# Kernel optimization log

Measured on AMD Instinct MI355X. Metric: run time of the kernel, lower is better.

## Reference

```python
import jax, jax.numpy as jnp
import numpy as np

B, S, E, H, F, V = 4, 2048, 1024, 16, 4096, 32000
D = E // H  # head_dim = 64
LN_EPS = 1e-5


def layer_norm(x, g, b):
    mu = jnp.mean(x, axis=-1, keepdims=True)
    var = jnp.mean(jnp.square(x - mu), axis=-1, keepdims=True)
    return (x - mu) * jax.lax.rsqrt(var + LN_EPS) * g + b


def setup_inputs() -> dict:
    key = jax.random.key(0)
    ks = jax.random.split(key, 12)
    s = 0.02
    return {
        "input_ids": jax.random.randint(ks[0], (B, S), 0, V),
        "attention_mask": jnp.ones((B, S), dtype=jnp.int32),
        "emb_table": jax.random.normal(ks[1], (V, E), jnp.float32) * s,
        "Wq": jax.random.normal(ks[2], (E, E), jnp.float32) * s,
        "bq": jnp.zeros((E,), jnp.float32),
        "Wk": jax.random.normal(ks[3], (E, E), jnp.float32) * s,
        "bk": jnp.zeros((E,), jnp.float32),
        "Wv": jax.random.normal(ks[4], (E, E), jnp.float32) * s,
        "bv": jnp.zeros((E,), jnp.float32),
        "Wo": jax.random.normal(ks[5], (E, E), jnp.float32) * s,
        "bo": jnp.zeros((E,), jnp.float32),
        "ln_g": jnp.ones((E,), jnp.float32),
        "ln_b": jnp.zeros((E,), jnp.float32),
        "W1": jax.random.normal(ks[6], (E, F), jnp.float32) * s,
        "b1": jnp.zeros((F,), jnp.float32),
        "W2": jax.random.normal(ks[7], (F, E), jnp.float32) * s,
        "b2": jnp.zeros((E,), jnp.float32),
        "Wp": jax.random.normal(ks[8], (E, 3), jnp.float32) * s,
        "bp": jnp.zeros((3,), jnp.float32),
    }


def reference(input_ids, attention_mask, emb_table, Wq, bq, Wk, bk, Wv, bv,
              Wo, bo, ln_g, ln_b, W1, b1, W2, b2, Wp, bp):
    b, s = input_ids.shape
    x = emb_table[input_ids]                                  # [B,S,E]
    q = (x @ Wq + bq).reshape(b, s, H, D).transpose(0, 2, 1, 3)  # [B,H,S,D]
    k = (x @ Wk + bk).reshape(b, s, H, D).transpose(0, 2, 1, 3)
    v = (x @ Wv + bv).reshape(b, s, H, D).transpose(0, 2, 1, 3)
    scores = jnp.einsum('bhqd,bhkd->bhqk', q, k) / jnp.sqrt(jnp.float32(D))
    mask = attention_mask[:, None, None, :]                   # [B,1,1,S]
    scores = jnp.where(mask == 0, -jnp.inf, scores)
    attn = jax.nn.softmax(scores, axis=-1)
    ctx = jnp.einsum('bhqk,bhkd->bhqd', attn, v)              # [B,H,S,D]
    ctx = ctx.transpose(0, 2, 1, 3).reshape(b, s, E)
    ctx = ctx @ Wo + bo
    h = layer_norm(ctx + x, ln_g, ln_b)
    ff = jax.nn.gelu(h @ W1 + b1, approximate=False) @ W2 + b2
    logits = ff @ Wp + bp                                     # [B,S,3]
    return logits.mean(axis=1)                                # [B,3]
```

## Files before the change

### kernel.cpp

```cpp
#include <hip/hip_runtime.h>
#include <hip/hip_bf16.h>
#include <math.h>

#define BB 4
#define SS 2048
#define EE 1024
#define HH 16
#define DD 64
#define FF 4096

typedef unsigned short u16;
typedef unsigned int u32;
typedef __bf16 bf16x8 __attribute__((ext_vector_type(8)));
typedef float f32x4 __attribute__((ext_vector_type(4)));

static __device__ __forceinline__ float gelu_exact(float v){
  return 0.5f * v * (1.0f + erff(v * 0.70710678118654752f));
}

static __device__ __forceinline__ u16 f2bf(float f){
  union { float f; u32 u; } x; x.f = f;
  u32 r = x.u + 0x7FFFu + ((x.u >> 16) & 1u);
  return (u16)(r >> 16);
}
static __device__ __forceinline__ void unpack2(u32 u, float& lo, float& hi){
  union { u32 u; float f; } a, b;
  a.u = u << 16; b.u = u & 0xFFFF0000u;
  lo = a.f; hi = b.f;
}

#define GLOAD_LDS16(g, l) \
  __builtin_amdgcn_global_load_lds((const __attribute__((address_space(1))) void*)(g), \
      (__attribute__((address_space(3))) void*)(l), 16, 0, 0)

__global__ __launch_bounds__(256) void embed_kernel(const int* __restrict__ ids,
    const float* __restrict__ emb, float* __restrict__ xf, u16* __restrict__ xbf){
  int row = blockIdx.x;
  int id  = ids[row];
  float4 v = ((const float4*)(emb + (size_t)id * EE))[threadIdx.x];
  ((float4*)(xf + (size_t)row * EE))[threadIdx.x] = v;
  ushort4 u; u.x = f2bf(v.x); u.y = f2bf(v.y); u.z = f2bf(v.z); u.w = f2bf(v.w);
  ((ushort4*)(xbf + (size_t)row * EE))[threadIdx.x] = u;
}

__global__ __launch_bounds__(256) void prep_weights(const float* __restrict__ Wq,
    const float* __restrict__ Wk, const float* __restrict__ Wv,
    const float* __restrict__ Wo, const float* __restrict__ W1, u16* __restrict__ WT){
  __shared__ float tile[32][33];
  int bid = blockIdx.x;
  const float* W; u16* dst; int N, n0, k0;
  if (bid < 4096){
    W = W1; dst = WT + (size_t)4 * EE * EE; N = FF;
    n0 = (bid & 127) * 32; k0 = (bid >> 7) * 32;
  } else {
    int idx = bid - 4096;
    int which = idx >> 10, t = idx & 1023;
    W = (which == 0) ? Wq : (which == 1) ? Wk : (which == 2) ? Wv : Wo;
    dst = WT + (size_t)which * EE * EE; N = EE;
    n0 = (t & 31) * 32; k0 = (t >> 5) * 32;
  }
  int tx = threadIdx.x & 31, ty = threadIdx.x >> 5;
  #pragma unroll
  for (int i = 0; i < 4; i++)
    tile[ty + 8*i][tx] = W[(size_t)(k0 + ty + 8*i) * N + n0 + tx];
  __syncthreads();
  #pragma unroll
  for (int i = 0; i < 4; i++)
    dst[(size_t)(n0 + ty + 8*i) * EE + k0 + tx] = f2bf(tile[tx][ty + 8*i]);
}

template<int MODE>
__global__ __launch_bounds__(256) void gemm_mfma(const u16* __restrict__ A,
    const u16* __restrict__ WT, const float* __restrict__ bias,
    const float* __restrict__ biasB, const float* __restrict__ biasC,
    u16* __restrict__ C, float* __restrict__ gsum, int M, int N, int K){
  __shared__ __attribute__((aligned(16))) u16 As[128 * 32];
  __shared__ __attribute__((aligned(16))) u16 Bs[128 * 32];

  const int tid = threadIdx.x;
  const int l = tid & 63, w = tid >> 6;
  const int lm = l & 15, lq = l >> 4;
  const int wm = (w >> 1) * 64, wn = (w & 1) * 64;
  const int r0 = blockIdx.y * 128, c0 = blockIdx.x * 128;

  const int srow0 = w * 32 + (l >> 2);
  const int scol  = (l & 3) * 8;
  const u16* Ab = A  + (size_t)(r0 + srow0) * K + scol;
  const u16* Bb = WT + (size_t)(c0 + srow0) * K + scol;
  u16* AsBase0 = &As[(w * 2)     * 512];
  u16* AsBase1 = &As[(w * 2 + 1) * 512];
  u16* BsBase0 = &Bs[(w * 2)     * 512];
  u16* BsBase1 = &Bs[(w * 2 + 1) * 512];

  f32x4 acc[4][4];
  const f32x4 zero = {0.f, 0.f, 0.f, 0.f};
  #pragma unroll
  for (int mi = 0; mi < 4; mi++)
    #pragma unroll
    for (int ni = 0; ni < 4; ni++) acc[mi][ni] = zero;

  for (int k0 = 0; k0 < K; k0 += 32){
    GLOAD_LDS16(Ab + k0,                    AsBase0);
    GLOAD_LDS16(Ab + (size_t)16 * K + k0,   AsBase1);
    GLOAD_LDS16(Bb + k0,                    BsBase0);
    GLOAD_LDS16(Bb + (size_t)16 * K + k0,   BsBase1);
    __syncthreads();

    bf16x8 af[4], bf[4];
    #pragma unroll
    for (int mi = 0; mi < 4; mi++)
      af[mi] = *(const bf16x8*)&As[(wm + mi*16 + lm) * 32 + lq * 8];
    #pragma unroll
    for (int ni = 0; ni < 4; ni++)
      bf[ni] = *(const bf16x8*)&Bs[(wn + ni*16 + lm) * 32 + lq * 8];
    #pragma unroll
    for (int mi = 0; mi < 4; mi++)
      #pragma unroll
      for (int ni = 0; ni < 4; ni++)
        acc[mi][ni] = __builtin_amdgcn_mfma_f32_16x16x32_bf16(af[mi], bf[ni], acc[mi][ni], 0, 0, 0);
    __syncthreads();
  }

  if constexpr (MODE == 0){
    #pragma unroll
    for (int ni = 0; ni < 4; ni++){
      int col = c0 + wn + ni*16 + lm;
      float bcol = bias[col];
      #pragma unroll
      for (int mi = 0; mi < 4; mi++){
        #pragma unroll
        for (int r = 0; r < 4; r++){
          int row = r0 + wm + mi*16 + lq*4 + r;
          C[(size_t)row * N + col] = f2bf(acc[mi][ni][r] + bcol);
        }
      }
    }
  } else if constexpr (MODE == 2){
    #pragma unroll
    for (int ni = 0; ni < 4; ni++){
      int col3 = c0 + wn + ni*16 + lm;
      int sel  = col3 >> 10;
      int colm = col3 & 1023;
      const float* bp_ = (sel == 0) ? bias : ((sel == 1) ? biasB : biasC);
      float bcol = bp_[colm];
      u16* dst = C + (size_t)sel * ((size_t)M * N);
      #pragma unroll
      for (int mi = 0; mi < 4; mi++){
        #pragma unroll
        for (int r = 0; r < 4; r++){
          int row = r0 + wm + mi*16 + lq*4 + r;
          dst[(size_t)row * N + colm] = f2bf(acc[mi][ni][r] + bcol);
        }
      }
    }
  } else {
    const int batch = r0 >> 11;
    #pragma unroll
    for (int ni = 0; ni < 4; ni++){
      int col = c0 + wn + ni*16 + lm;
      float bcol = bias[col];
      float cs = 0.f;
      #pragma unroll
      for (int mi = 0; mi < 4; mi++)
        #pragma unroll
        for (int r = 0; r < 4; r++)
          cs += gelu_exact(acc[mi][ni][r] + bcol);
      cs += __shfl_xor(cs, 16, 64);
      cs += __shfl_xor(cs, 32, 64);
      if (lq == 0) atomicAdd(&gsum[(size_t)batch * N + col], cs);
    }
  }
}

__global__ __launch_bounds__(256, 4) void attn_mfma(const u16* __restrict__ q,
    const u16* __restrict__ k, const u16* __restrict__ v,
    const int* __restrict__ mask, u16* __restrict__ ctx){
  const int bh = blockIdx.y, b = bh >> 4, h = bh & 15;
  const int q0 = blockIdx.x * 128;
  const int tid = threadIdx.x;
  const int w = tid >> 6, l = tid & 63, lm = l & 15, lq = l >> 4;

  __shared__ __attribute__((aligned(16))) u16 Kt[64 * 72];
  __shared__ __attribute__((aligned(16))) u16 Vt[64 * 72];
  __shared__ __attribute__((aligned(16))) u16 Pw[4][32 * 72];
  __shared__ float mb[64];

  bf16x8 aq[2][2];
  #pragma unroll
  for (int mg = 0; mg < 2; mg++){
    const u16* qrow = q + (size_t)(b*SS + q0 + w*32 + mg*16 + lm) * EE + h*DD + lq*8;
    aq[mg][0] = *(const bf16x8*)qrow;
    aq[mg][1] = *(const bf16x8*)(qrow + 32);
  }

  f32x4 occ[2][4];
  const f32x4 zero = {0.f,0.f,0.f,0.f};
  #pragma unroll
  for (int mg = 0; mg < 2; mg++)
    #pragma unroll
    for (int ni = 0; ni < 4; ni++) occ[mg][ni] = zero;
  float l_part[2][4] = {{0.f,0.f,0.f,0.f},{0.f,0.f,0.f,0.f}};

  const int kkey = tid >> 2, kc16 = (tid & 3) * 16;
  const u16* kbase = k + (size_t)(b*SS + kkey) * EE + h*DD + kc16;
  const int kp = tid & 31, vd0 = (tid >> 5) * 8;
  const u16* vbase0 = v + (size_t)(b*SS + 2*kp) * EE + h*DD + vd0;
  const u16* vbase1 = vbase0 + EE;

  uint4 kr0 = *(const uint4*)(kbase);
  uint4 kr1 = *(const uint4*)(kbase + 8);
  uint4 vr0 = *(const uint4*)(vbase0);
  uint4 vr1 = *(const uint4*)(vbase1);
  float mreg = 0.f;
  if (tid < 64) mreg = (mask[b*SS + tid] != 0) ? 0.f : -1e30f;

  const float SCALE_LOG2E = 0.125f * 1.4426950408889634f;

  for (int t0 = 0; t0 < SS; t0 += 64){
    *(uint4*)&Kt[kkey*72 + kc16]     = kr0;
    *(uint4*)&Kt[kkey*72 + kc16 + 8] = kr1;
    {
      union { uint4 u; u16 s[8]; } va, vb;
      va.u = vr0; vb.u = vr1;
      #pragma unroll
      for (int i = 0; i < 8; i++){
        u32 pk = (u32)va.s[i] | ((u32)vb.s[i] << 16);
        *(u32*)&Vt[(vd0 + i)*72 + 2*kp] = pk;
      }
    }
    if (tid < 64) mb[tid] = mreg;
    __syncthreads();

    if (t0 + 64 < SS){
      kr0 = *(const uint4*)(kbase + (size_t)(t0 + 64) * EE);
      kr1 = *(const uint4*)(kbase + (size_t)(t0 + 64) * EE + 8);
      vr0 = *(const uint4*)(vbase0 + (size_t)(t0 + 64) * EE);
      vr1 = *(const uint4*)(vbase1 + (size_t)(t0 + 64) * EE);
      if (tid < 64) mreg = (mask[b*SS + t0 + 64 + tid] != 0) ? 0.f : -1e30f;
    }

    #pragma unroll
    for (int mg = 0; mg < 2; mg++){
      #pragma unroll
      for (int ni = 0; ni < 4; ni++){
        bf16x8 b0 = *(const bf16x8*)&Kt[(ni*16 + lm)*72 + lq*8];
        bf16x8 b1 = *(const bf16x8*)&Kt[(ni*16 + lm)*72 + 32 + lq*8];
        f32x4 sc = zero;
        sc = __builtin_amdgcn_mfma_f32_16x16x32_bf16(aq[mg][0], b0, sc, 0, 0, 0);
        sc = __builtin_amdgcn_mfma_f32_16x16x32_bf16(aq[mg][1], b1, sc, 0, 0, 0);
        float mbias = mb[ni*16 + lm];
        #pragma unroll
        for (int r = 0; r < 4; r++){
          float s = fminf(fmaf(sc[r], SCALE_LOG2E, mbias), 80.f);
          float p = __builtin_amdgcn_exp2f(s);
          l_part[mg][r] += p;
          Pw[w][(mg*16 + lq*4 + r)*72 + ni*16 + lm] = f2bf(p);
        }
      }
    }
    bf16x8 ap[2][2];
    #pragma unroll
    for (int mg = 0; mg < 2; mg++){
      ap[mg][0] = *(const bf16x8*)&Pw[w][(mg*16 + lm)*72 + lq*8];
      ap[mg][1] = *(const bf16x8*)&Pw[w][(mg*16 + lm)*72 + 32 + lq*8];
    }

    #pragma unroll
    for (int ni = 0; ni < 4; ni++){
      bf16x8 vb0 = *(const bf16x8*)&Vt[(ni*16 + lm)*72 + lq*8];
      bf16x8 vb1 = *(const bf16x8*)&Vt[(ni*16 + lm)*72 + 32 + lq*8];
      #pragma unroll
      for (int mg = 0; mg < 2; mg++){
        occ[mg][ni] = __builtin_amdgcn_mfma_f32_16x16x32_bf16(ap[mg][0], vb0, occ[mg][ni], 0, 0, 0);
        occ[mg][ni] = __builtin_amdgcn_mfma_f32_16x16x32_bf16(ap[mg][1], vb1, occ[mg][ni], 0, 0, 0);
      }
    }
    __syncthreads();
  }

  #pragma unroll
  for (int mg = 0; mg < 2; mg++){
    float inv[4];
    #pragma unroll
    for (int r = 0; r < 4; r++){
      float s = l_part[mg][r];
      s += __shfl_xor(s, 1, 64);
      s += __shfl_xor(s, 2, 64);
      s += __shfl_xor(s, 4, 64);
      s += __shfl_xor(s, 8, 64);
      inv[r] = 1.f / s;
    }
    #pragma unroll
    for (int ni = 0; ni < 4; ni++){
      int col = h*DD + ni*16 + lm;
      #pragma unroll
      for (int r = 0; r < 4; r++){
        int row = q0 + w*32 + mg*16 + lq*4 + r;
        ctx[(size_t)(b*SS + row) * EE + col] = f2bf(occ[mg][ni][r] * inv[r]);
      }
    }
  }
}

__global__ __launch_bounds__(256) void ln_kernel(const u16* __restrict__ c2,
    const float* __restrict__ x, const float* __restrict__ g,
    const float* __restrict__ bta, u16* __restrict__ h){
  int row = blockIdx.x, tid = threadIdx.x;
  uint2 cu = ((const uint2*)(c2 + (size_t)row * EE))[tid];
  float c0,c1,c2f,c3;
  unpack2(cu.x, c0, c1); unpack2(cu.y, c2f, c3);
  float4 xv = ((const float4*)(x + (size_t)row * EE))[tid];
  float4 y = make_float4(c0+xv.x, c1+xv.y, c2f+xv.z, c3+xv.w);
  float s  = y.x + y.y + y.z + y.w;
  float ss = y.x*y.x + y.y*y.y + y.z*y.z + y.w*y.w;
  #pragma unroll
  for (int off=32; off; off>>=1){
    s  += __shfl_xor(s,  off, 64);
    ss += __shfl_xor(ss, off, 64);
  }
  __shared__ float rs[4], rss[4];
  int w = tid >> 6;
  if ((tid & 63) == 0){ rs[w] = s; rss[w] = ss; }
  __syncthreads();
  float tot  = rs[0]+rs[1]+rs[2]+rs[3];
  float tots = rss[0]+rss[1]+rss[2]+rss[3];
  float mu  = tot  * (1.f/EE);
  float var = tots * (1.f/EE) - mu*mu;
  float inv = rsqrtf(var + 1e-5f);
  float4 gv = ((const float4*)g)[tid];
  float4 bv = ((const float4*)bta)[tid];
  ushort4 ou;
  ou.x = f2bf((y.x-mu)*inv*gv.x + bv.x);
  ou.y = f2bf((y.y-mu)*inv*gv.y + bv.y);
  ou.z = f2bf((y.z-mu)*inv*gv.z + bv.z);
  ou.w = f2bf((y.w-mu)*inv*gv.w + bv.w);
  ((ushort4*)(h + (size_t)row * EE))[tid] = ou;
}

__global__ __launch_bounds__(256) void w2wp_kernel(const float* __restrict__ W2,
    const float* __restrict__ Wp, float* __restrict__ W2Wp){
  int f0 = blockIdx.x * 8;
  int tid = threadIdx.x;
  int e0 = tid * 4;
  float wp[4][3];
  #pragma unroll
  for (int t = 0; t < 4; t++)
    #pragma unroll
    for (int j = 0; j < 3; j++) wp[t][j] = Wp[(e0 + t)*3 + j];
  __shared__ float red[3][4];
  for (int i = 0; i < 8; i++){
    int f = f0 + i;
    float4 wv = ((const float4*)(W2 + (size_t)f * EE))[tid];
    float w4[4] = {wv.x, wv.y, wv.z, wv.w};
    float p[3] = {0.f, 0.f, 0.f};
    #pragma unroll
    for (int t = 0; t < 4; t++)
      #pragma unroll
      for (int j = 0; j < 3; j++) p[j] += w4[t] * wp[t][j];
    #pragma unroll
    for (int j = 0; j < 3; j++){
      float sj = p[j];
      #pragma unroll
      for (int off = 32; off; off >>= 1) sj += __shfl_xor(sj, off, 64);
      if ((tid & 63) == 0) red[j][tid >> 6] = sj;
    }
    __syncthreads();
    if (tid < 3) W2Wp[f*3 + tid] = red[tid][0] + red[tid][1] + red[tid][2] + red[tid][3];
    __syncthreads();
  }
}

__global__ __launch_bounds__(256) void out_final(const float* __restrict__ gsum,
    const float* __restrict__ W2Wp, const float* __restrict__ b2,
    const float* __restrict__ Wp, const float* __restrict__ bp, float* __restrict__ out){
  int tid = threadIdx.x;
  float part[4][3];
  #pragma unroll
  for (int b = 0; b < 4; b++)
    #pragma unroll
    for (int j = 0; j < 3; j++) part[b][j] = 0.f;
  for (int f = tid; f < FF; f += 256){
    float w0 = W2Wp[f*3], w1 = W2Wp[f*3+1], w2v = W2Wp[f*3+2];
    #pragma unroll
    for (int b = 0; b < 4; b++){
      float g = gsum[b*FF + f] * (1.f/SS);
      part[b][0] += g * w0; part[b][1] += g * w1; part[b][2] += g * w2v;
    }
  }
  float bb[3] = {0.f, 0.f, 0.f};
  for (int e = tid; e < EE; e += 256){
    float bv = b2[e];
    bb[0] += bv * Wp[e*3]; bb[1] += bv * Wp[e*3+1]; bb[2] += bv * Wp[e*3+2];
  }
  __shared__ float red[15][4];
  int lane = tid & 63, w = tid >> 6;
  #pragma unroll
  for (int b = 0; b < 4; b++)
    #pragma unroll
    for (int j = 0; j < 3; j++){
      float s = part[b][j];
      #pragma unroll
      for (int off = 32; off; off >>= 1) s += __shfl_xor(s, off, 64);
      if (lane == 0) red[b*3 + j][w] = s;
    }
  #pragma unroll
  for (int j = 0; j < 3; j++){
    float s = bb[j];
    #pragma unroll
    for (int off = 32; off; off >>= 1) s += __shfl_xor(s, off, 64);
    if (lane == 0) red[12 + j][w] = s;
  }
  __syncthreads();
  if (tid < 12){
    int j = tid % 3;
    float s  = red[tid][0] + red[tid][1] + red[tid][2] + red[tid][3];
    float bj = red[12+j][0] + red[12+j][1] + red[12+j][2] + red[12+j][3];
    out[tid] = s + bj + bp[j];
  }
}

extern "C" void kernel_launch(void* const* d_in, const int* in_sizes, int n_in,
                              void* d_out, int out_size, void* d_ws, size_t ws_size,
                              hipStream_t stream) {
  const int M = BB * SS;
  const int* ids  = (const int*)d_in[0];
  const int* mask = (const int*)d_in[1];
  const float* emb = (const float*)d_in[2];
  const float* Wq = (const float*)d_in[3];  const float* bq = (const float*)d_in[4];
  const float* Wk = (const float*)d_in[5];  const float* bk = (const float*)d_in[6];
  const float* Wv = (const float*)d_in[7];  const float* bv = (const float*)d_in[8];
  const float* Wo = (const float*)d_in[9];  const float* bo = (const float*)d_in[10];
  const float* lg = (const float*)d_in[11]; const float* lb = (const float*)d_in[12];
  const float* W1 = (const float*)d_in[13]; const float* b1 = (const float*)d_in[14];
  const float* W2 = (const float*)d_in[15]; const float* b2 = (const float*)d_in[16];
  const float* Wp = (const float*)d_in[17]; const float* bp = (const float*)d_in[18];

  char* base = (char*)d_ws;
  const size_t SLOTF = (size_t)M * EE;
  float* xf   = (float*)base;
  u16*  xbf   = (u16*)(base + SLOTF*4);
  u16*  qbf   = (u16*)(base + SLOTF*6);
  u16*  kbf   = (u16*)(base + SLOTF*8);
  u16*  vbf   = (u16*)(base + SLOTF*10);
  u16*  ctxbf = (u16*)(base + SLOTF*12);
  u16*  c2bf  = qbf;
  u16*  hbf   = kbf;
  u16*  WqT   = (u16*)(base + SLOTF*14);
  u16*  W1T   = WqT + (size_t)4*EE*EE;
  float* gsum = (float*)(W1T + (size_t)FF*EE);
  float* w2wp = gsum + BB*FF;

  hipMemsetAsync(gsum, 0, BB*FF*sizeof(float), stream);

  embed_kernel<<<M, 256, 0, stream>>>(ids, emb, xf, xbf);

  prep_weights<<<8192, 256, 0, stream>>>(Wq, Wk, Wv, Wo, W1, WqT);
  w2wp_kernel<<<FF/8, 256, 0, stream>>>(W2, Wp, w2wp);

  gemm_mfma<2><<<dim3(3*EE/128, M/128), 256, 0, stream>>>(
      xbf, WqT, bq, bk, bv, qbf, nullptr, M, EE, EE);

  attn_mfma<<<dim3(SS/128, BB*HH), 256, 0, stream>>>(qbf, kbf, vbf, mask, ctxbf);

  gemm_mfma<0><<<dim3(EE/128, M/128), 256, 0, stream>>>(
      ctxbf, WqT + (size_t)3*EE*EE, bo, nullptr, nullptr, c2bf, nullptr, M, EE, EE);

  ln_kernel<<<M, 256, 0, stream>>>(c2bf, xf, lg, lb, hbf);

  gemm_mfma<1><<<dim3(FF/128, M/128), 256, 0, stream>>>(
      hbf, W1T, b1, nullptr, nullptr, nullptr, gsum, M, FF, EE);

  out_final<<<1, 256, 0, stream>>>(gsum, w2wp, b2, Wp, bp, (float*)d_out);
}
```

Before: 625.0 us.

## Double-buffer GEMM and attention LDS tiles, load A and K fragments directly

The GEMM now keeps a double-buffered B tile in LDS with one barrier per k-step, and loads A fragments straight from global memory into registers with a one-step prefetch. The attention kernel loads K MFMA fragments directly from global memory, double-buffers V and the mask bias in LDS to drop the trailing barrier, and removes the occupancy hint from its launch bounds. This is meant to cut LDS traffic and barriers and to overlap loads with MFMA work. The cost is uncoalesced, latency-exposed global loads for A and K fragments, plus more register pressure.

```diff
diff --git a/kernel.cpp b/kernel.cpp
--- a/kernel.cpp
+++ b/kernel.cpp
@@ -74,8 +74,7 @@
     const u16* __restrict__ WT, const float* __restrict__ bias,
     const float* __restrict__ biasB, const float* __restrict__ biasC,
     u16* __restrict__ C, float* __restrict__ gsum, int M, int N, int K){
-  __shared__ __attribute__((aligned(16))) u16 As[128 * 32];
-  __shared__ __attribute__((aligned(16))) u16 Bs[128 * 32];
+  __shared__ __attribute__((aligned(16))) u16 Bs[2][128 * 32];
 
   const int tid = threadIdx.x;
   const int l = tid & 63, w = tid >> 6;
@@ -85,12 +84,8 @@
 
   const int srow0 = w * 32 + (l >> 2);
   const int scol  = (l & 3) * 8;
-  const u16* Ab = A  + (size_t)(r0 + srow0) * K + scol;
   const u16* Bb = WT + (size_t)(c0 + srow0) * K + scol;
-  u16* AsBase0 = &As[(w * 2)     * 512];
-  u16* AsBase1 = &As[(w * 2 + 1) * 512];
-  u16* BsBase0 = &Bs[(w * 2)     * 512];
-  u16* BsBase1 = &Bs[(w * 2 + 1) * 512];
+  const u16* Ab = A  + (size_t)(r0 + wm + lm) * K + lq * 8;
 
   f32x4 acc[4][4];
   const f32x4 zero = {0.f, 0.f, 0.f, 0.f};
@@ -99,26 +94,36 @@
     #pragma unroll
     for (int ni = 0; ni < 4; ni++) acc[mi][ni] = zero;
 
-  for (int k0 = 0; k0 < K; k0 += 32){
-    GLOAD_LDS16(Ab + k0,                    AsBase0);
-    GLOAD_LDS16(Ab + (size_t)16 * K + k0,   AsBase1);
-    GLOAD_LDS16(Bb + k0,                    BsBase0);
-    GLOAD_LDS16(Bb + (size_t)16 * K + k0,   BsBase1);
+  bf16x8 acur[4], anext[4];
+  #pragma unroll
+  for (int mi = 0; mi < 4; mi++)
+    acur[mi] = *(const bf16x8*)(Ab + (size_t)(mi * 16) * K);
+  GLOAD_LDS16(Bb,                  &Bs[0][(w * 2)     * 512]);
+  GLOAD_LDS16(Bb + (size_t)16 * K, &Bs[0][(w * 2 + 1) * 512]);
+
+  const int NIT = K / 32;
+  for (int it = 0; it < NIT; it++){
     __syncthreads();
-
-    bf16x8 af[4], bf[4];
+    if (it + 1 < NIT){
+      GLOAD_LDS16(Bb + (size_t)(it + 1) * 32,
+                  &Bs[(it + 1) & 1][(w * 2)     * 512]);
+      GLOAD_LDS16(Bb + (size_t)16 * K + (size_t)(it + 1) * 32,
+                  &Bs[(it + 1) & 1][(w * 2 + 1) * 512]);
+      #pragma unroll
+      for (int mi = 0; mi < 4; mi++)
+        anext[mi] = *(const bf16x8*)(Ab + (size_t)(mi * 16) * K + (size_t)(it + 1) * 32);
+    }
+    bf16x8 bf[4];
+    #pragma unroll
+    for (int ni = 0; ni < 4; ni++)
+      bf[ni] = *(const bf16x8*)&Bs[it & 1][(wn + ni*16 + lm) * 32 + lq * 8];
     #pragma unroll
     for (int mi = 0; mi < 4; mi++)
-      af[mi] = *(const bf16x8*)&As[(wm + mi*16 + lm) * 32 + lq * 8];
-    #pragma unroll
-    for (int ni = 0; ni < 4; ni++)
-      bf[ni] = *(const bf16x8*)&Bs[(wn + ni*16 + lm) * 32 + lq * 8];
-    #pragma unroll
-    for (int mi = 0; mi < 4; mi++)
       #pragma unroll
       for (int ni = 0; ni < 4; ni++)
-        acc[mi][ni] = __builtin_amdgcn_mfma_f32_16x16x32_bf16(af[mi], bf[ni], acc[mi][ni], 0, 0, 0);
-    __syncthreads();
+        acc[mi][ni] = __builtin_amdgcn_mfma_f32_16x16x32_bf16(acur[mi], bf[ni], acc[mi][ni], 0, 0, 0);
+    #pragma unroll
+    for (int mi = 0; mi < 4; mi++) acur[mi] = anext[mi];
   }
 
   if constexpr (MODE == 0){
@@ -172,7 +177,7 @@
   }
 }
 
-__global__ __launch_bounds__(256, 4) void attn_mfma(const u16* __restrict__ q,
+__global__ __launch_bounds__(256) void attn_mfma(const u16* __restrict__ q,
     const u16* __restrict__ k, const u16* __restrict__ v,
     const int* __restrict__ mask, u16* __restrict__ ctx){
   const int bh = blockIdx.y, b = bh >> 4, h = bh & 15;
@@ -180,10 +185,9 @@
   const int tid = threadIdx.x;
   const int w = tid >> 6, l = tid & 63, lm = l & 15, lq = l >> 4;
 
-  __shared__ __attribute__((aligned(16))) u16 Kt[64 * 72];
-  __shared__ __attribute__((aligned(16))) u16 Vt[64 * 72];
+  __shared__ __attribute__((aligned(16))) u16 Vt[2][64 * 72];
   __shared__ __attribute__((aligned(16))) u16 Pw[4][32 * 72];
-  __shared__ float mb[64];
+  __shared__ float mb[2][64];
 
   bf16x8 aq[2][2];
   #pragma unroll
@@ -201,54 +205,55 @@
     for (int ni = 0; ni < 4; ni++) occ[mg][ni] = zero;
   float l_part[2][4] = {{0.f,0.f,0.f,0.f},{0.f,0.f,0.f,0.f}};
 
-  const int kkey = tid >> 2, kc16 = (tid & 3) * 16;
-  const u16* kbase = k + (size_t)(b*SS + kkey) * EE + h*DD + kc16;
   const int kp = tid & 31, vd0 = (tid >> 5) * 8;
   const u16* vbase0 = v + (size_t)(b*SS + 2*kp) * EE + h*DD + vd0;
   const u16* vbase1 = vbase0 + EE;
-
-  uint4 kr0 = *(const uint4*)(kbase);
-  uint4 kr1 = *(const uint4*)(kbase + 8);
+  const u16* kfbase = k + (size_t)(b*SS + lm) * EE + h*DD + lq*8;
+
   uint4 vr0 = *(const uint4*)(vbase0);
   uint4 vr1 = *(const uint4*)(vbase1);
   float mreg = 0.f;
   if (tid < 64) mreg = (mask[b*SS + tid] != 0) ? 0.f : -1e30f;
 
   const float SCALE_LOG2E = 0.125f * 1.4426950408889634f;
-
-  for (int t0 = 0; t0 < SS; t0 += 64){
-    *(uint4*)&Kt[kkey*72 + kc16]     = kr0;
-    *(uint4*)&Kt[kkey*72 + kc16 + 8] = kr1;
+  const int NT = SS / 64;
+
+  for (int it = 0; it < NT; it++){
+    const int t0 = it * 64;
     {
-      union { uint4 u; u16 s[8]; } va, vb;
-      va.u = vr0; vb.u = vr1;
+      union { uint4 u; u16 s[8]; } va, vb_;
+      va.u = vr0; vb_.u = vr1;
       #pragma unroll
       for (int i = 0; i < 8; i++){
-        u32 pk = (u32)va.s[i] | ((u32)vb.s[i] << 16);
-        *(u32*)&Vt[(vd0 + i)*72 + 2*kp] = pk;
-      }
-    }
-    if (tid < 64) mb[tid] = mreg;
+        u32 pk = (u32)va.s[i] | ((u32)vb_.s[i] << 16);
+        *(u32*)&Vt[it & 1][(vd0 + i)*72 + 2*kp] = pk;
+      }
+    }
+    if (tid < 64) mb[it & 1][tid] = mreg;
     __syncthreads();
 
-    if (t0 + 64 < SS){
-      kr0 = *(const uint4*)(kbase + (size_t)(t0 + 64) * EE);
-      kr1 = *(const uint4*)(kbase + (size_t)(t0 + 64) * EE + 8);
+    if (it + 1 < NT){
       vr0 = *(const uint4*)(vbase0 + (size_t)(t0 + 64) * EE);
       vr1 = *(const uint4*)(vbase1 + (size_t)(t0 + 64) * EE);
       if (tid < 64) mreg = (mask[b*SS + t0 + 64 + tid] != 0) ? 0.f : -1e30f;
     }
 
+    bf16x8 kf0[4], kf1[4];
+    #pragma unroll
+    for (int ni = 0; ni < 4; ni++){
+      const u16* kr = kfbase + (size_t)(t0 + ni*16) * EE;
+      kf0[ni] = *(const bf16x8*)kr;
+      kf1[ni] = *(const bf16x8*)(kr + 32);
+    }
+
     #pragma unroll
     for (int mg = 0; mg < 2; mg++){
       #pragma unroll
       for (int ni = 0; ni < 4; ni++){
-        bf16x8 b0 = *(const bf16x8*)&Kt[(ni*16 + lm)*72 + lq*8];
-        bf16x8 b1 = *(const bf16x8*)&Kt[(ni*16 + lm)*72 + 32 + lq*8];
         f32x4 sc = zero;
-        sc = __builtin_amdgcn_mfma_f32_16x16x32_bf16(aq[mg][0], b0, sc, 0, 0, 0);
-        sc = __builtin_amdgcn_mfma_f32_16x16x32_bf16(aq[mg][1], b1, sc, 0, 0, 0);
-        float mbias = mb[ni*16 + lm];
+        sc = __builtin_amdgcn_mfma_f32_16x16x32_bf16(aq[mg][0], kf0[ni], sc, 0, 0, 0);
+        sc = __builtin_amdgcn_mfma_f32_16x16x32_bf16(aq[mg][1], kf1[ni], sc, 0, 0, 0);
+        float mbias = mb[it & 1][ni*16 + lm];
         #pragma unroll
         for (int r = 0; r < 4; r++){
           float s = fminf(fmaf(sc[r], SCALE_LOG2E, mbias), 80.f);
@@ -267,15 +272,14 @@
 
     #pragma unroll
     for (int ni = 0; ni < 4; ni++){
-      bf16x8 vb0 = *(const bf16x8*)&Vt[(ni*16 + lm)*72 + lq*8];
-      bf16x8 vb1 = *(const bf16x8*)&Vt[(ni*16 + lm)*72 + 32 + lq*8];
+      bf16x8 vb0 = *(const bf16x8*)&Vt[it & 1][(ni*16 + lm)*72 + lq*8];
+      bf16x8 vb1 = *(const bf16x8*)&Vt[it & 1][(ni*16 + lm)*72 + 32 + lq*8];
       #pragma unroll
       for (int mg = 0; mg < 2; mg++){
         occ[mg][ni] = __builtin_amdgcn_mfma_f32_16x16x32_bf16(ap[mg][0], vb0, occ[mg][ni], 0, 0, 0);
         occ[mg][ni] = __builtin_amdgcn_mfma_f32_16x16x32_bf16(ap[mg][1], vb1, occ[mg][ni], 0, 0, 0);
       }
     }
-    __syncthreads();
   }
 
   #pragma unroll
```

Measured after the change: 784.8 us. +25.6%, slower.
